# Performance work log

Measured on AMD Instinct MI355X. Metric: run time of the kernel, lower is better.

The kernel has to match this reference:

```python
import jax, jax.numpy as jnp
import numpy as np

BRANCH, DEPTH = 10, 3          # balanced hierarchy: 10^3 = 1000 leaf classes
NUM_CLASSES = BRANCH ** DEPTH
NUM_EDGES = DEPTH
N_TOKENS = 32768
IGNORE_INDEX = -100


def _build_tree_tensors():
    """Reproduce HierarchicalLLLoss.__init__ for a balanced tree.

    For leaf i, its ancestor edge at level j (j=0 is the leaf's own edge)
    spans the contiguous leaf block of size BRANCH**j containing i.
    """
    C, E = NUM_CLASSES, NUM_EDGES
    onehot_num = np.zeros((C, C, E), np.float32)
    onehot_den = np.zeros((C, C, E), np.float32)
    weights = np.zeros((C, E), np.float32)
    leaves = np.arange(C)
    cols = np.arange(C)
    for j in range(E):
        s_num = BRANCH ** j
        start_num = (leaves // s_num) * s_num              # [C]
        mask_num = (cols[None, :] >= start_num[:, None]) & (cols[None, :] < (start_num + s_num)[:, None])
        onehot_num[:, :, j] = mask_num.astype(np.float32)
        s_den = BRANCH ** (j + 1)                          # parent subtree; top level -> all ones
        start_den = (leaves // s_den) * s_den
        mask_den = (cols[None, :] >= start_den[:, None]) & (cols[None, :] < (start_den + s_den)[:, None])
        onehot_den[:, :, j] = mask_den.astype(np.float32)
        weights[:, j] = np.exp(-0.5 * j)                   # edge weight by height above leaf
    return onehot_num, onehot_den, weights


def setup_inputs() -> dict:
    key = jax.random.key(0)
    k1, k2 = jax.random.split(key)
    onehot_num, onehot_den, weights = _build_tree_tensors()
    # class "probabilities" (positive; normalization cancels in the num/den ratio)
    inputs = jax.random.uniform(k1, (N_TOKENS, NUM_CLASSES), jnp.float32, 1e-4, 1.0)
    target = jax.random.randint(k2, (N_TOKENS,), 0, NUM_CLASSES, dtype=jnp.int64)
    return {
        "inputs": inputs,
        "target": target,
        "onehot_num": jnp.asarray(onehot_num),
        "onehot_den": jnp.asarray(onehot_den),
        "weights": jnp.asarray(weights),
    }


def reference(inputs, target, onehot_num, onehot_den, weights):
    valid = target != IGNORE_INDEX                          # [N] bool
    t = jnp.where(valid, target, 0)                          # safe gather index
    # bmm of [N,1,C] with gathered [N,C,E] -> [N,E]
    num = jnp.einsum("nc,nce->ne", inputs, onehot_num[t])
    den = jnp.einsum("nc,nce->ne", inputs, onehot_den[t])
    nz = num != 0
    num = jnp.where(nz, -jnp.log(num / jnp.where(nz, den, 1.0)), num)
    # flip does not change the sum but is kept for fidelity to the source
    per_tok = jnp.sum(jnp.flip(weights[t] * num, axis=1), axis=1)  # [N]
    per_tok = jnp.where(valid, per_tok, 0.0)
    count = jnp.maximum(jnp.sum(valid.astype(jnp.float32)), 1.0)
    return jnp.sum(per_tok) / count
```

## Files before the change

### kernel.cpp

```cpp
#include <hip/hip_runtime.h>
#include <math.h>

#define N_TOKENS     32768
#define NUM_CLASSES  1000
#define IGNORE_INDEX (-100)
#define TOK_PER_BLK  4
#define NBLOCKS      (N_TOKENS / TOK_PER_BLK)

__global__ __launch_bounds__(256) void hll_partial(
    const float* __restrict__ inputs,
    const int*   __restrict__ target,
    const float* __restrict__ weights,
    float* __restrict__ partial_sum,
    float* __restrict__ partial_cnt)
{
    const int wave = threadIdx.x >> 6;
    const int lane = threadIdx.x & 63;
    const int n = blockIdx.x * TOK_PER_BLK + wave;

    const int t = target[n];
    const bool valid = (t != IGNORE_INDEX);
    const int tt = valid ? t : 0;
    const int lo1 = (tt / 10) * 10;
    const int lo2 = (tt / 100) * 100;

    const float* __restrict__ rowp = inputs + (size_t)n * NUM_CLASSES;
    const float4* __restrict__ row = reinterpret_cast<const float4*>(rowp);

    float s3 = 0.f;
    #pragma unroll
    for (int i = 0; i < 4; ++i) {
        const int idx4 = i * 64 + lane;
        if (idx4 < NUM_CLASSES / 4) {
            const float4 v = row[idx4];
            s3 += (v.x + v.y) + (v.z + v.w);
        }
    }

    float s2 = 0.f;
    if (lane < 25) {
        const float4 v = row[lo2 / 4 + lane];
        s2 = (v.x + v.y) + (v.z + v.w);
    }
    float s1 = (lane < 10) ? rowp[lo1 + lane] : 0.f;
    const float s0 = rowp[tt];

    #pragma unroll
    for (int off = 32; off >= 1; off >>= 1) {
        s3 += __shfl_down(s3, off, 64);
        s2 += __shfl_down(s2, off, 64);
        s1 += __shfl_down(s1, off, 64);
    }

    __shared__ float red_loss[TOK_PER_BLK];
    __shared__ float red_cnt[TOK_PER_BLK];
    if (lane == 0) {
        float loss = 0.f;
        if (valid) {
            const float w0 = weights[tt * 3 + 0];
            const float w1 = weights[tt * 3 + 1];
            const float w2 = weights[tt * 3 + 2];
            const float l0 = (s0 != 0.f) ? -logf(s0 / s1) : 0.f;
            const float l1 = (s1 != 0.f) ? -logf(s1 / s2) : 0.f;
            const float l2 = (s2 != 0.f) ? -logf(s2 / s3) : 0.f;
            loss = w0 * l0 + w1 * l1 + w2 * l2;
        }
        red_loss[wave] = loss;
        red_cnt[wave]  = valid ? 1.f : 0.f;
    }
    __syncthreads();
    if (threadIdx.x == 0) {
        float ls = 0.f, cs = 0.f;
        #pragma unroll
        for (int w = 0; w < TOK_PER_BLK; ++w) { ls += red_loss[w]; cs += red_cnt[w]; }
        partial_sum[blockIdx.x] = ls;
        partial_cnt[blockIdx.x] = cs;
    }
}

__global__ __launch_bounds__(256) void hll_final(
    const float4* __restrict__ partial_sum4,
    const float4* __restrict__ partial_cnt4,
    float* __restrict__ out)
{
    const int wave = threadIdx.x >> 6;
    const int lane = threadIdx.x & 63;
    float s = 0.f, c = 0.f;
    for (int i = threadIdx.x; i < NBLOCKS / 4; i += 256) {
        const float4 a = partial_sum4[i];
        const float4 b = partial_cnt4[i];
        s += (a.x + a.y) + (a.z + a.w);
        c += (b.x + b.y) + (b.z + b.w);
    }
    #pragma unroll
    for (int off = 32; off >= 1; off >>= 1) {
        s += __shfl_down(s, off, 64);
        c += __shfl_down(c, off, 64);
    }
    __shared__ float ssum[4], scnt[4];
    if (lane == 0) { ssum[wave] = s; scnt[wave] = c; }
    __syncthreads();
    if (threadIdx.x == 0) {
        const float S  = ssum[0] + ssum[1] + ssum[2] + ssum[3];
        const float Ct = scnt[0] + scnt[1] + scnt[2] + scnt[3];
        out[0] = S / fmaxf(Ct, 1.0f);
    }
}

extern "C" void kernel_launch(void* const* d_in, const int* in_sizes, int n_in,
                              void* d_out, int out_size, void* d_ws, size_t ws_size,
                              hipStream_t stream) {
    const float* inputs  = (const float*)d_in[0];
    const int*   target  = (const int*)d_in[1];
    const float* weights = (const float*)d_in[4];
    float* out = (float*)d_out;

    float* partial_sum = (float*)d_ws;
    float* partial_cnt = partial_sum + NBLOCKS;

    hll_partial<<<NBLOCKS, 256, 0, stream>>>(inputs, target, weights,
                                             partial_sum, partial_cnt);
    hll_final<<<1, 256, 0, stream>>>((const float4*)partial_sum,
                                     (const float4*)partial_cnt, out);
}
```

Baseline: 204.9 us.

## Fuse final reduction via last-block ticket and process four tokens per wave

Merges the partial and final kernels into one launch: each block publishes a packed (sum,count) partial, bumps an atomic ticket, and the last block to arrive performs the global reduction. Each wave now handles four tokens in sequence, so the grid shrinks to 2048 blocks. This removes the second kernel launch and its dependency gap, but adds a memset launch for the ticket plus atomics, and lowers the number of loads in flight per wave unless the compiler overlaps the unrolled token iterations.

```diff
diff --git a/kernel.cpp b/kernel.cpp
--- a/kernel.cpp
+++ b/kernel.cpp
@@ -4,106 +4,110 @@
 #define N_TOKENS     32768
 #define NUM_CLASSES  1000
 #define IGNORE_INDEX (-100)
-#define TOK_PER_BLK  4
-#define NBLOCKS      (N_TOKENS / TOK_PER_BLK)
+#define NBLOCKS      2048
+#define WAVES_PER_BLK 4
+#define TOK_PER_WAVE 4
 
-__global__ __launch_bounds__(256) void hll_partial(
+typedef unsigned long long u64;
+union PackF2 { u64 u; struct { float s, c; } f; };
+
+__global__ __launch_bounds__(256) void hll_fused(
     const float* __restrict__ inputs,
     const int*   __restrict__ target,
     const float* __restrict__ weights,
-    float* __restrict__ partial_sum,
-    float* __restrict__ partial_cnt)
+    unsigned int* __restrict__ ticket,
+    u64* __restrict__ partials,
+    float* __restrict__ out)
 {
     const int wave = threadIdx.x >> 6;
     const int lane = threadIdx.x & 63;
-    const int n = blockIdx.x * TOK_PER_BLK + wave;
+    const int gw = blockIdx.x * WAVES_PER_BLK + wave;
 
-    const int t = target[n];
-    const bool valid = (t != IGNORE_INDEX);
-    const int tt = valid ? t : 0;
-    const int lo1 = (tt / 10) * 10;
-    const int lo2 = (tt / 100) * 100;
-
-    const float* __restrict__ rowp = inputs + (size_t)n * NUM_CLASSES;
-    const float4* __restrict__ row = reinterpret_cast<const float4*>(rowp);
-
-    float s3 = 0.f;
-    #pragma unroll
-    for (int i = 0; i < 4; ++i) {
-        const int idx4 = i * 64 + lane;
-        if (idx4 < NUM_CLASSES / 4) {
-            const float4 v = row[idx4];
-            s3 += (v.x + v.y) + (v.z + v.w);
-        }
-    }
-
-    float s2 = 0.f;
-    if (lane < 25) {
-        const float4 v = row[lo2 / 4 + lane];
-        s2 = (v.x + v.y) + (v.z + v.w);
-    }
-    float s1 = (lane < 10) ? rowp[lo1 + lane] : 0.f;
-    const float s0 = rowp[tt];
+    float wave_loss = 0.f, wave_cnt = 0.f;
 
     #pragma unroll
-    for (int off = 32; off >= 1; off >>= 1) {
-        s3 += __shfl_down(s3, off, 64);
-        s2 += __shfl_down(s2, off, 64);
-        s1 += __shfl_down(s1, off, 64);
-    }
+    for (int k = 0; k < TOK_PER_WAVE; ++k) {
+        const int n = gw * TOK_PER_WAVE + k;
+        const int t = target[n];
+        const bool valid = (t != IGNORE_INDEX);
+        const int tt = valid ? t : 0;
+        const int lo1 = (tt / 10) * 10;
+        const int lo2 = (tt / 100) * 100;
+        const float* __restrict__ rowp = inputs + (size_t)n * NUM_CLASSES;
+        const float4* __restrict__ row = (const float4*)rowp;
 
-    __shared__ float red_loss[TOK_PER_BLK];
-    __shared__ float red_cnt[TOK_PER_BLK];
-    if (lane == 0) {
-        float loss = 0.f;
-        if (valid) {
+        float s3 = 0.f;
+        #pragma unroll
+        for (int i = 0; i < 4; ++i) {
+            const int idx4 = i * 64 + lane;
+            if (idx4 < NUM_CLASSES / 4) {
+                const float4 v = row[idx4];
+                s3 += (v.x + v.y) + (v.z + v.w);
+            }
+        }
+        float s2 = 0.f;
+        if (lane < 25) {
+            const float4 v = row[lo2 / 4 + lane];
+            s2 = (v.x + v.y) + (v.z + v.w);
+        }
+        float s1 = (lane < 10) ? rowp[lo1 + lane] : 0.f;
+        const float s0 = rowp[tt];
+
+        #pragma unroll
+        for (int off = 32; off >= 1; off >>= 1) {
+            s3 += __shfl_down(s3, off, 64);
+            s2 += __shfl_down(s2, off, 64);
+            s1 += __shfl_down(s1, off, 64);
+        }
+        if (lane == 0 && valid) {
             const float w0 = weights[tt * 3 + 0];
             const float w1 = weights[tt * 3 + 1];
             const float w2 = weights[tt * 3 + 2];
             const float l0 = (s0 != 0.f) ? -logf(s0 / s1) : 0.f;
             const float l1 = (s1 != 0.f) ? -logf(s1 / s2) : 0.f;
             const float l2 = (s2 != 0.f) ? -logf(s2 / s3) : 0.f;
-            loss = w0 * l0 + w1 * l1 + w2 * l2;
+            wave_loss += w0 * l0 + w1 * l1 + w2 * l2;
+            wave_cnt  += 1.f;
         }
-        red_loss[wave] = loss;
-        red_cnt[wave]  = valid ? 1.f : 0.f;
+    }
+
+    __shared__ float rl[WAVES_PER_BLK], rc[WAVES_PER_BLK];
+    __shared__ unsigned int last_flag;
+    if (lane == 0) { rl[wave] = wave_loss; rc[wave] = wave_cnt; }
+    __syncthreads();
+    if (threadIdx.x == 0) {
+        PackF2 p;
+        p.f.s = (rl[0] + rl[1]) + (rl[2] + rl[3]);
+        p.f.c = (rc[0] + rc[1]) + (rc[2] + rc[3]);
+        __hip_atomic_store(&partials[blockIdx.x], p.u,
+                           __ATOMIC_RELAXED, __HIP_MEMORY_SCOPE_AGENT);
+        const unsigned int tk = __hip_atomic_fetch_add(
+            ticket, 1u, __ATOMIC_ACQ_REL, __HIP_MEMORY_SCOPE_AGENT);
+        last_flag = (tk == (unsigned)(gridDim.x - 1)) ? 1u : 0u;
     }
     __syncthreads();
-    if (threadIdx.x == 0) {
-        float ls = 0.f, cs = 0.f;
+    if (last_flag) {
+        float s = 0.f, c = 0.f;
         #pragma unroll
-        for (int w = 0; w < TOK_PER_BLK; ++w) { ls += red_loss[w]; cs += red_cnt[w]; }
-        partial_sum[blockIdx.x] = ls;
-        partial_cnt[blockIdx.x] = cs;
-    }
-}
-
-__global__ __launch_bounds__(256) void hll_final(
-    const float4* __restrict__ partial_sum4,
-    const float4* __restrict__ partial_cnt4,
-    float* __restrict__ out)
-{
-    const int wave = threadIdx.x >> 6;
-    const int lane = threadIdx.x & 63;
-    float s = 0.f, c = 0.f;
-    for (int i = threadIdx.x; i < NBLOCKS / 4; i += 256) {
-        const float4 a = partial_sum4[i];
-        const float4 b = partial_cnt4[i];
-        s += (a.x + a.y) + (a.z + a.w);
-        c += (b.x + b.y) + (b.z + b.w);
-    }
-    #pragma unroll
-    for (int off = 32; off >= 1; off >>= 1) {
-        s += __shfl_down(s, off, 64);
-        c += __shfl_down(c, off, 64);
-    }
-    __shared__ float ssum[4], scnt[4];
-    if (lane == 0) { ssum[wave] = s; scnt[wave] = c; }
-    __syncthreads();
-    if (threadIdx.x == 0) {
-        const float S  = ssum[0] + ssum[1] + ssum[2] + ssum[3];
-        const float Ct = scnt[0] + scnt[1] + scnt[2] + scnt[3];
-        out[0] = S / fmaxf(Ct, 1.0f);
+        for (int r = 0; r < NBLOCKS / 256; ++r) {
+            PackF2 p;
+            p.u = __hip_atomic_load(&partials[r * 256 + threadIdx.x],
+                                    __ATOMIC_RELAXED, __HIP_MEMORY_SCOPE_AGENT);
+            s += p.f.s; c += p.f.c;
+        }
+        #pragma unroll
+        for (int off = 32; off >= 1; off >>= 1) {
+            s += __shfl_down(s, off, 64);
+            c += __shfl_down(c, off, 64);
+        }
+        __shared__ float fs[WAVES_PER_BLK], fc[WAVES_PER_BLK];
+        if (lane == 0) { fs[wave] = s; fc[wave] = c; }
+        __syncthreads();
+        if (threadIdx.x == 0) {
+            const float S  = (fs[0] + fs[1]) + (fs[2] + fs[3]);
+            const float Ct = (fc[0] + fc[1]) + (fc[2] + fc[3]);
+            out[0] = S / fmaxf(Ct, 1.0f);
+        }
     }
 }
 
@@ -115,11 +119,10 @@
     const float* weights = (const float*)d_in[4];
     float* out = (float*)d_out;
 
-    float* partial_sum = (float*)d_ws;
-    float* partial_cnt = partial_sum + NBLOCKS;
+    unsigned int* ticket = (unsigned int*)d_ws;
+    u64* partials = (u64*)((char*)d_ws + 16);
 
-    hll_partial<<<NBLOCKS, 256, 0, stream>>>(inputs, target, weights,
-                                             partial_sum, partial_cnt);
-    hll_final<<<1, 256, 0, stream>>>((const float4*)partial_sum,
-                                     (const float4*)partial_cnt, out);
+    hipMemsetAsync(ticket, 0, sizeof(unsigned int), stream);
+    hll_fused<<<NBLOCKS, 256, 0, stream>>>(inputs, target, weights,
+                                           ticket, partials, out);
 }
```

After: 245.1 us. 1.2x slower.
